# Optimization experiments

Measured on AMD Instinct MI355X. Metric: run time of the kernel, lower is better.

The kernel has to match this reference:

```python
import jax, jax.numpy as jnp
import numpy as np

V, C, T, H, L, B = 32000, 1024, 1024, 16, 8, 4
HS = C // H
STD = 0.02


def _layernorm(x, g, b, eps=1e-5):
    m = jnp.mean(x, axis=-1, keepdims=True)
    v = jnp.mean(jnp.square(x - m), axis=-1, keepdims=True)
    return (x - m) * jax.lax.rsqrt(v + eps) * g + b


def setup_inputs() -> dict:
    key = jax.random.key(0)
    ks = jax.random.split(key, 16)
    n = lambda k, shape: (jax.random.normal(k, shape, dtype=jnp.float32) * STD)
    return {
        "index": jax.random.randint(ks[0], (B, T), 0, V),
        "targets": jax.random.randint(ks[1], (B, T), 0, V),
        "tok_emb": n(ks[2], (V, C)),
        "pos_emb": n(ks[3], (T, C)),
        "wq": n(ks[4], (L, C, C)),
        "wk": n(ks[5], (L, C, C)),
        "wv": n(ks[6], (L, C, C)),
        "wo": n(ks[7], (L, C, C)),
        "bo": jnp.zeros((L, C), jnp.float32),
        "w1": n(ks[8], (L, C, 4 * C)),
        "b1": jnp.zeros((L, 4 * C), jnp.float32),
        "w2": n(ks[9], (L, 4 * C, C)),
        "b2": jnp.zeros((L, C), jnp.float32),
        "ln1_g": jnp.ones((L, C), jnp.float32),
        "ln1_b": jnp.zeros((L, C), jnp.float32),
        "ln2_g": jnp.ones((L, C), jnp.float32),
        "ln2_b": jnp.zeros((L, C), jnp.float32),
        "lnf_g": jnp.ones((C,), jnp.float32),
        "lnf_b": jnp.zeros((C,), jnp.float32),
        "lm_w": n(ks[10], (C, V)),
        "lm_b": jnp.zeros((V,), jnp.float32),
    }


def reference(index, targets, tok_emb, pos_emb, wq, wk, wv, wo, bo, w1, b1, w2,
              b2, ln1_g, ln1_b, ln2_g, ln2_b, lnf_g, lnf_b, lm_w, lm_b):
    b, t = index.shape
    x = tok_emb[index] + pos_emb[:t]                      # [B,T,C]
    causal = jnp.tril(jnp.ones((t, t), dtype=bool))       # tril mask
    scale = HS ** -0.5
    for l in range(L):  # fixed small layer loop
        q = (x @ wq[l]).reshape(b, t, H, HS)
        k = (x @ wk[l]).reshape(b, t, H, HS)
        v = (x @ wv[l]).reshape(b, t, H, HS)
        scores = jnp.einsum('bqhd,bkhd->bhqk', q, k) * scale
        scores = jnp.where(causal, scores, -jnp.inf)
        w = jax.nn.softmax(scores, axis=-1)               # dropout p=0 -> identity
        att = jnp.einsum('bhqk,bkhd->bqhd', w, v).reshape(b, t, C)
        x = _layernorm(x + att @ wo[l] + bo[l], ln1_g[l], ln1_b[l])
        h = jax.nn.relu(x @ w1[l] + b1[l])
        x = _layernorm(x + h @ w2[l] + b2[l], ln2_g[l], ln2_b[l])
    x = _layernorm(x, lnf_g, lnf_b)
    logits = (x @ lm_w + lm_b).reshape(b * t, V)
    logp = jax.nn.log_softmax(logits, axis=-1)
    loss = -jnp.take_along_axis(logp, targets.reshape(-1, 1), axis=1).mean()
    return logits, loss
```

## Files before the change

### kernel.cpp

```cpp
#include <hip/hip_runtime.h>

typedef unsigned short u16;
typedef __attribute__((ext_vector_type(4))) float f32x4;
typedef __attribute__((ext_vector_type(8))) short s16x8;
typedef __attribute__((ext_vector_type(4))) short s16x4;

static constexpr int V = 32000;
static constexpr int C = 1024;
static constexpr int T = 1024;
static constexpr int H = 16;
static constexpr int L = 8;
static constexpr int B = 4;
static constexpr int HS = 64;
static constexpr int BT = B * T;
static constexpr int C4 = 4 * C;
static constexpr int C3 = 3 * C;

__device__ __forceinline__ u16 f2bf(float f) {
  union { float f; unsigned u; } v; v.f = f;
  unsigned r = v.u + 0x7fffu + ((v.u >> 16) & 1u);
  return (u16)(r >> 16);
}

__device__ __forceinline__ void gload16(const u16* g, u16* l) {
  __builtin_amdgcn_global_load_lds(
      (const __attribute__((address_space(1))) void*)g,
      (__attribute__((address_space(3))) void*)l, 16, 0, 0);
}

__device__ __forceinline__ float blockReduceSum(float v) {
  __shared__ float red[4];
  int lane = threadIdx.x & 63, w = threadIdx.x >> 6;
#pragma unroll
  for (int m = 32; m >= 1; m >>= 1) v += __shfl_xor(v, m, 64);
  if (lane == 0) red[w] = v;
  __syncthreads();
  float r = red[0] + red[1] + red[2] + red[3];
  __syncthreads();
  return r;
}

__global__ __launch_bounds__(256) void k_embed(
    const int* __restrict__ idx, const float* __restrict__ tok,
    const float* __restrict__ pos, float* __restrict__ x, u16* __restrict__ xb) {
  int bt = blockIdx.x;
  int t = bt & (T - 1);
  int row = idx[bt];
  const float* te = tok + (size_t)row * C;
  const float* pe = pos + (size_t)t * C;
  float* xo = x + (size_t)bt * C;
  u16* xbo = xb + (size_t)bt * C;
  for (int c = threadIdx.x; c < C; c += 256) {
    float v = te[c] + pe[c];
    xo[c] = v;
    xbo[c] = f2bf(v);
  }
}

__global__ __launch_bounds__(256) void k_transpose(
    const float* __restrict__ W, u16* __restrict__ Wt, int K, int N,
    size_t sW, size_t sWt) {
  __shared__ float tile[64][65];
  const float* Wz = W + sW * blockIdx.z;
  u16* Wtz = Wt + sWt * blockIdx.z;
  int n0 = blockIdx.x * 64, k0 = blockIdx.y * 64;
  int tc = threadIdx.x & 63, tr = threadIdx.x >> 6;
#pragma unroll
  for (int i = 0; i < 16; ++i) {
    int r = tr + i * 4;
    tile[r][tc] = Wz[(size_t)(k0 + r) * N + (n0 + tc)];
  }
  __syncthreads();
#pragma unroll
  for (int i = 0; i < 16; ++i) {
    int r = tr + i * 4;
    Wtz[(size_t)(n0 + r) * K + (k0 + tc)] = f2bf(tile[tc][r]);
  }
}

template <int OUT_BF16, int RELU, int HAS_BIAS, int HAS_RES>
__global__ __launch_bounds__(256, 2) void k_gemm(
    const u16* __restrict__ A, const u16* __restrict__ Bt,
    const float* __restrict__ bias, const float* __restrict__ Res,
    float* __restrict__ Cf, u16* __restrict__ Cb, int M, int N, int K) {
  __shared__ u16 As[128 * 32];
  __shared__ u16 Bs[128 * 32];
  int tid = threadIdx.x;
  int lane = tid & 63, wid = tid >> 6;
  int lm = lane & 15, lg = lane >> 4;
  int wm = wid >> 1, wn = wid & 1;

  unsigned nbx = gridDim.x;
  unsigned nwg = nbx * gridDim.y;
  unsigned orig = blockIdx.y * nbx + blockIdx.x;
  unsigned f = ((nwg & 7u) == 0u) ? (orig & 7u) * (nwg >> 3) + (orig >> 3) : orig;
  int mb = (int)(f / nbx) * 128, nb = (int)(f % nbx) * 128;

  f32x4 acc[4][4];
#pragma unroll
  for (int i = 0; i < 4; ++i)
#pragma unroll
    for (int j = 0; j < 4; ++j) acc[i][j] = f32x4{0.f, 0.f, 0.f, 0.f};

  int r0 = tid >> 2, q0 = tid & 3;
  int r1 = (256 + tid) >> 2, q1 = tid & 3;
  const u16* a0 = A + (size_t)(mb + r0) * K + q0 * 8;
  const u16* a1 = A + (size_t)(mb + r1) * K + q1 * 8;
  const u16* b0 = Bt + (size_t)(nb + r0) * K + q0 * 8;
  const u16* b1 = Bt + (size_t)(nb + r1) * K + q1 * 8;
  u16* lA0 = &As[wid * 512];
  u16* lA1 = &As[2048 + wid * 512];
  u16* lB0 = &Bs[wid * 512];
  u16* lB1 = &Bs[2048 + wid * 512];

  int nK = K >> 5;
  for (int kb = 0; kb < nK; ++kb) {
    __syncthreads();
    int ko = kb * 32;
    gload16(a0 + ko, lA0);
    gload16(a1 + ko, lA1);
    gload16(b0 + ko, lB0);
    gload16(b1 + ko, lB1);
    __syncthreads();
    s16x8 af[4], bfr[4];
#pragma unroll
    for (int m = 0; m < 4; ++m)
      af[m] = *(const s16x8*)&As[(wm * 64 + m * 16 + lm) * 32 + lg * 8];
#pragma unroll
    for (int n = 0; n < 4; ++n)
      bfr[n] = *(const s16x8*)&Bs[(wn * 64 + n * 16 + lm) * 32 + lg * 8];
#pragma unroll
    for (int m = 0; m < 4; ++m)
#pragma unroll
      for (int n = 0; n < 4; ++n)
        acc[m][n] = __builtin_amdgcn_mfma_f32_16x16x32_bf16(af[m], bfr[n],
                                                            acc[m][n], 0, 0, 0);
  }
#pragma unroll
  for (int m = 0; m < 4; ++m) {
#pragma unroll
    for (int n = 0; n < 4; ++n) {
      int col = nb + wn * 64 + n * 16 + lm;
      float bv = HAS_BIAS ? bias[col] : 0.0f;
#pragma unroll
      for (int r = 0; r < 4; ++r) {
        int row = mb + wm * 64 + m * 16 + lg * 4 + r;
        float v = acc[m][n][r] + bv;
        if (HAS_RES) v += Res[(size_t)row * N + col];
        if (RELU) v = v > 0.f ? v : 0.f;
        if (OUT_BF16)
          Cb[(size_t)row * N + col] = f2bf(v);
        else
          Cf[(size_t)row * N + col] = v;
      }
    }
  }
}

template <int OUT_BF16, int RELU, int HAS_BIAS, int HAS_RES, int VT, int LOSS>
__global__ __launch_bounds__(512) void k_gemm256(
    const u16* __restrict__ A, const u16* __restrict__ Bt,
    const float* __restrict__ bias, const float* __restrict__ Res,
    float* __restrict__ Cf, u16* __restrict__ Cb, u16* __restrict__ Vtp,
    float2* __restrict__ Pp, int M, int N, int K) {
  __shared__ u16 As[2][16384];
  __shared__ u16 Bs[2][16384];
  const int tid = threadIdx.x;
  const int lane = tid & 63, wid = tid >> 6;
  const int lm = lane & 15, lg = lane >> 4;
  const int wr = wid >> 2, wc = wid & 3;

  unsigned nbx = gridDim.x;
  unsigned nwg = nbx * gridDim.y;
  unsigned orig = blockIdx.y * nbx + blockIdx.x;
  unsigned f = ((nwg & 7u) == 0u) ? (orig & 7u) * (nwg >> 3) + (orig >> 3) : orig;
  const int mb = (int)(f / nbx) * 256, nb = (int)(f % nbx) * 256;

  int aoff[4], boff[4], ldso[4];
#pragma unroll
  for (int h = 0; h < 4; ++h) {
    const int kk = h >> 1, p = h & 1;
    int rem = p * 512 + tid;
    int rblk = rem >> 6;
    int rem2 = rem & 63;
    int row16 = rem2 >> 2, psl = rem2 & 3;
    int sl = psl ^ ((row16 >> 1) & 3);
    int grow = rblk * 16 + row16;
    int gk = kk * 32 + sl * 8;
    aoff[h] = (mb + grow) * K + gk;
    boff[h] = (nb + grow) * K + gk;
    ldso[h] = kk * 8192 + p * 4096 + wid * 512;
  }
  const int lo = lm * 32 + ((lg ^ ((lm >> 1) & 3)) << 3);

  f32x4 acc[8][4];
#pragma unroll
  for (int i = 0; i < 8; ++i)
#pragma unroll
    for (int j = 0; j < 4; ++j) acc[i][j] = f32x4{0.f, 0.f, 0.f, 0.f};

  const int nK = K >> 6;
  gload16(A + aoff[0], &As[0][ldso[0]]);
  gload16(A + aoff[1], &As[0][ldso[1]]);
  gload16(Bt + boff[0], &Bs[0][ldso[0]]);
  gload16(Bt + boff[1], &Bs[0][ldso[1]]);
  gload16(A + aoff[2], &As[0][ldso[2]]);
  gload16(A + aoff[3], &As[0][ldso[3]]);
  gload16(Bt + boff[2], &Bs[0][ldso[2]]);
  gload16(Bt + boff[3], &Bs[0][ldso[3]]);
  asm volatile("s_waitcnt vmcnt(4)" ::: "memory");
  __builtin_amdgcn_s_barrier();

  for (int t = 0; t < nK; ++t) {
    const int buf = t & 1, nbuf = buf ^ 1;
    const bool pre = (t + 1 < nK);
    const int nk64 = (t + 1) * 64;
    s16x8 af[4], bfr[4];
#pragma unroll
    for (int m = 0; m < 4; ++m)
      af[m] = *(const s16x8*)&As[buf][(wr * 8 + m) * 512 + lo];
#pragma unroll
    for (int n = 0; n < 4; ++n)
      bfr[n] = *(const s16x8*)&Bs[buf][(wc * 4 + n) * 512 + lo];
    if (pre) {
      gload16(A + aoff[0] + nk64, &As[nbuf][ldso[0]]);
      gload16(A + aoff[1] + nk64, &As[nbuf][ldso[1]]);
    }
    __builtin_amdgcn_s_barrier();
    __builtin_amdgcn_s_setprio(1);
#pragma unroll
    for (int m = 0; m < 4; ++m)
#pragma unroll
      for (int n = 0; n < 4; ++n)
        acc[m][n] = __builtin_amdgcn_mfma_f32_16x16x32_bf16(af[m], bfr[n],
                                                            acc[m][n], 0, 0, 0);
    __builtin_amdgcn_s_setprio(0);
    __builtin_amdgcn_s_barrier();
#pragma unroll
    for (int m = 0; m < 4; ++m)
      af[m] = *(const s16x8*)&As[buf][(wr * 8 + 4 + m) * 512 + lo];
    if (pre) {
      gload16(Bt + boff[0] + nk64, &Bs[nbuf][ldso[0]]);
      gload16(Bt + boff[1] + nk64, &Bs[nbuf][ldso[1]]);
    }
    __builtin_amdgcn_s_barrier();
    __builtin_amdgcn_s_setprio(1);
#pragma unroll
    for (int m = 0; m < 4; ++m)
#pragma unroll
      for (int n = 0; n < 4; ++n)
        acc[m + 4][n] = __builtin_amdgcn_mfma_f32_16x16x32_bf16(
            af[m], bfr[n], acc[m + 4][n], 0, 0, 0);
    __builtin_amdgcn_s_setprio(0);
    __builtin_amdgcn_s_barrier();
#pragma unroll
    for (int m = 0; m < 4; ++m)
      af[m] = *(const s16x8*)&As[buf][8192 + (wr * 8 + m) * 512 + lo];
#pragma unroll
    for (int n = 0; n < 4; ++n)
      bfr[n] = *(const s16x8*)&Bs[buf][8192 + (wc * 4 + n) * 512 + lo];
    if (pre) {
      gload16(A + aoff[2] + nk64, &As[nbuf][ldso[2]]);
      gload16(A + aoff[3] + nk64, &As[nbuf][ldso[3]]);
      asm volatile("s_waitcnt vmcnt(6)" ::: "memory");
    } else {
      asm volatile("s_waitcnt vmcnt(0)" ::: "memory");
    }
    __builtin_amdgcn_s_barrier();
    __builtin_amdgcn_s_setprio(1);
#pragma unroll
    for (int m = 0; m < 4; ++m)
#pragma unroll
      for (int n = 0; n < 4; ++n)
        acc[m][n] = __builtin_amdgcn_mfma_f32_16x16x32_bf16(af[m], bfr[n],
                                                            acc[m][n], 0, 0, 0);
    __builtin_amdgcn_s_setprio(0);
    __builtin_amdgcn_s_barrier();
#pragma unroll
    for (int m = 0; m < 4; ++m)
      af[m] = *(const s16x8*)&As[buf][8192 + (wr * 8 + 4 + m) * 512 + lo];
    if (pre) {
      gload16(Bt + boff[2] + nk64, &Bs[nbuf][ldso[2]]);
      gload16(Bt + boff[3] + nk64, &Bs[nbuf][ldso[3]]);
      asm volatile("s_waitcnt vmcnt(4)" ::: "memory");
    }
    __builtin_amdgcn_s_barrier();
    __builtin_amdgcn_s_setprio(1);
#pragma unroll
    for (int m = 0; m < 4; ++m)
#pragma unroll
      for (int n = 0; n < 4; ++n)
        acc[m + 4][n] = __builtin_amdgcn_mfma_f32_16x16x32_bf16(
            af[m], bfr[n], acc[m + 4][n], 0, 0, 0);
    __builtin_amdgcn_s_setprio(0);
    __builtin_amdgcn_s_barrier();
  }
  if (VT && nb >= 2 * C) {
    int hh = ((nb - 2 * C) >> 6) + wc;
#pragma unroll
    for (int m = 0; m < 8; ++m) {
      int t0 = mb + wr * 128 + m * 16 + lg * 4;
      int bb = t0 >> 10, tt = t0 & (T - 1);
      size_t vbase = ((size_t)(bb * H + hh) * HS) * T + tt;
#pragma unroll
      for (int n = 0; n < 4; ++n) {
        int d = n * 16 + lm;
        s16x4 pk;
#pragma unroll
        for (int r = 0; r < 4; ++r) pk[r] = (short)f2bf(acc[m][n][r]);
        *(s16x4*)&Vtp[vbase + (size_t)d * T] = pk;
      }
    }
    return;
  }
  float bv[4];
#pragma unroll
  for (int n = 0; n < 4; ++n)
    bv[n] = HAS_BIAS ? bias[nb + wc * 64 + n * 16 + lm] : 0.0f;
#pragma unroll
  for (int m = 0; m < 8; ++m) {
#pragma unroll
    for (int r = 0; r < 4; ++r) {
      int row = mb + wr * 128 + m * 16 + lg * 4 + r;
#pragma unroll
      for (int n = 0; n < 4; ++n) {
        int col = nb + wc * 64 + n * 16 + lm;
        float v = acc[m][n][r] + bv[n];
        if (HAS_RES) v += Res[(size_t)row * N + col];
        if (RELU) v = v > 0.f ? v : 0.f;
        if (OUT_BF16)
          Cb[(size_t)row * N + col] = f2bf(v);
        else
          Cf[(size_t)row * N + col] = v;
      }
    }
  }
  if (LOSS) {
    __syncthreads();
    float* red = (float*)&As[0][0];
    float Mx[8][4], Sx[8][4];
#pragma unroll
    for (int m = 0; m < 8; ++m)
#pragma unroll
      for (int r = 0; r < 4; ++r) {
        float v0 = acc[m][0][r] + bv[0];
        float v1 = acc[m][1][r] + bv[1];
        float v2 = acc[m][2][r] + bv[2];
        float v3 = acc[m][3][r] + bv[3];
        Mx[m][r] = fmaxf(fmaxf(v0, v1), fmaxf(v2, v3));
      }
#pragma unroll
    for (int d = 1; d < 16; d <<= 1)
#pragma unroll
      for (int m = 0; m < 8; ++m)
#pragma unroll
        for (int r = 0; r < 4; ++r)
          Mx[m][r] = fmaxf(Mx[m][r], __shfl_xor(Mx[m][r], d, 16));
    if (lm == 0) {
#pragma unroll
      for (int m = 0; m < 8; ++m)
#pragma unroll
        for (int r = 0; r < 4; ++r)
          red[(wr * 128 + m * 16 + lg * 4 + r) * 4 + wc] = Mx[m][r];
    }
    __syncthreads();
#pragma unroll
    for (int m = 0; m < 8; ++m)
#pragma unroll
      for (int r = 0; r < 4; ++r) {
        int rl = wr * 128 + m * 16 + lg * 4 + r;
        Mx[m][r] = fmaxf(fmaxf(red[rl * 4 + 0], red[rl * 4 + 1]),
                         fmaxf(red[rl * 4 + 2], red[rl * 4 + 3]));
      }
    __syncthreads();
#pragma unroll
    for (int m = 0; m < 8; ++m)
#pragma unroll
      for (int r = 0; r < 4; ++r)
        Sx[m][r] = __expf(acc[m][0][r] + bv[0] - Mx[m][r]) +
                   __expf(acc[m][1][r] + bv[1] - Mx[m][r]) +
                   __expf(acc[m][2][r] + bv[2] - Mx[m][r]) +
                   __expf(acc[m][3][r] + bv[3] - Mx[m][r]);
#pragma unroll
    for (int d = 1; d < 16; d <<= 1)
#pragma unroll
      for (int m = 0; m < 8; ++m)
#pragma unroll
        for (int r = 0; r < 4; ++r)
          Sx[m][r] += __shfl_xor(Sx[m][r], d, 16);
    if (lm == 0) {
#pragma unroll
      for (int m = 0; m < 8; ++m)
#pragma unroll
        for (int r = 0; r < 4; ++r)
          red[(wr * 128 + m * 16 + lg * 4 + r) * 4 + wc] = Sx[m][r];
    }
    __syncthreads();
    if (wc == 0 && lm == 0) {
      int nblk = nb >> 8;
#pragma unroll
      for (int m = 0; m < 8; ++m)
#pragma unroll
        for (int r = 0; r < 4; ++r) {
          int rl = wr * 128 + m * 16 + lg * 4 + r;
          float ss = red[rl * 4 + 0] + red[rl * 4 + 1] + red[rl * 4 + 2] +
                     red[rl * 4 + 3];
          Pp[(size_t)(mb + rl) * 128 + nblk] = float2{Mx[m][r], ss};
        }
    }
  }
}

__global__ __launch_bounds__(256) void k_attn(
    const u16* __restrict__ qkv, const u16* __restrict__ vt,
    u16* __restrict__ o) {
  constexpr int PP = 72;
  __shared__ u16 Ks[64 * 64];
  __shared__ u16 Vs[64 * 64];
  __shared__ u16 Ps[4][16 * PP];
  int bid = blockIdx.x;
  int p = bid & 7, h = (bid >> 3) & 15, b = bid >> 7;
  int tid = threadIdx.x, lane = tid & 63, wid = tid >> 6;
  int lm = lane & 15, lg = lane >> 4;
  const size_t rowbase = (size_t)b * T * C3 + (size_t)h * HS;
  const u16* kbase = qkv + rowbase + C;
  const u16* vbase = vt + (size_t)(b * H + h) * HS * T;
  const size_t obase = (size_t)b * T * C + (size_t)h * HS;
  const float scale = 0.125f;
  const int sr = tid >> 3, scs = (tid & 7) ^ (sr & 7);
  const int swz0 = (lg ^ (lm & 7)) * 8;
  const int swz1 = ((4 + lg) ^ (lm & 7)) * 8;

  for (int qi = 0; qi < 2; ++qi) {
    int qt = qi ? (15 - p) : p;
    int qw = qt * 64 + wid * 16;
    s16x8 qf[2];
#pragma unroll
    for (int s = 0; s < 2; ++s)
      qf[s] = *(const s16x8*)&qkv[rowbase + (size_t)(qw + lm) * C3 + s * 32 +
                                  lg * 8];
    float m_[4], l_[4];
    f32x4 oacc[4];
#pragma unroll
    for (int r = 0; r < 4; ++r) { m_[r] = -3e38f; l_[r] = 0.f; }
#pragma unroll
    for (int n = 0; n < 4; ++n) oacc[n] = f32x4{0.f, 0.f, 0.f, 0.f};

    for (int kt = 0; kt <= qt; ++kt) {
      __syncthreads();
      gload16(kbase + (size_t)(kt * 64 + sr) * C3 + scs * 8, &Ks[wid * 512]);
      gload16(kbase + (size_t)(kt * 64 + sr + 32) * C3 + scs * 8,
              &Ks[2048 + wid * 512]);
      gload16(vbase + (size_t)sr * T + kt * 64 + scs * 8, &Vs[wid * 512]);
      gload16(vbase + (size_t)(sr + 32) * T + kt * 64 + scs * 8,
              &Vs[2048 + wid * 512]);
      __syncthreads();

      f32x4 s[4];
#pragma unroll
      for (int ch = 0; ch < 4; ++ch) {
        s16x8 k0 = *(const s16x8*)&Ks[(ch * 16 + lm) * 64 + swz0];
        s16x8 k1 = *(const s16x8*)&Ks[(ch * 16 + lm) * 64 + swz1];
        s[ch] = f32x4{0.f, 0.f, 0.f, 0.f};
        s[ch] = __builtin_amdgcn_mfma_f32_16x16x32_bf16(qf[0], k0, s[ch], 0, 0, 0);
        s[ch] = __builtin_amdgcn_mfma_f32_16x16x32_bf16(qf[1], k1, s[ch], 0, 0, 0);
      }
      if (kt == qt) {
#pragma unroll
        for (int ch = 0; ch < 4; ++ch) {
          int col = kt * 64 + ch * 16 + lm;
#pragma unroll
          for (int r = 0; r < 4; ++r) {
            int row = qw + lg * 4 + r;
            s[ch][r] = (col <= row) ? s[ch][r] * scale : -3e38f;
          }
        }
      } else {
#pragma unroll
        for (int ch = 0; ch < 4; ++ch)
#pragma unroll
          for (int r = 0; r < 4; ++r) s[ch][r] *= scale;
      }
      float rmax[4];
#pragma unroll
      for (int r = 0; r < 4; ++r)
        rmax[r] = fmaxf(fmaxf(s[0][r], s[1][r]), fmaxf(s[2][r], s[3][r]));
#pragma unroll
      for (int mm = 1; mm < 16; mm <<= 1)
#pragma unroll
        for (int r = 0; r < 4; ++r)
          rmax[r] = fmaxf(rmax[r], __shfl_xor(rmax[r], mm, 16));
      float alpha[4], rsum[4];
#pragma unroll
      for (int r = 0; r < 4; ++r) {
        float mn = fmaxf(m_[r], rmax[r]);
        alpha[r] = __expf(m_[r] - mn);
        m_[r] = mn;
        rsum[r] = 0.f;
      }
#pragma unroll
      for (int ch = 0; ch < 4; ++ch)
#pragma unroll
        for (int r = 0; r < 4; ++r) {
          float e = __expf(s[ch][r] - m_[r]);
          s[ch][r] = e;
          rsum[r] += e;
        }
#pragma unroll
      for (int mm = 1; mm < 16; mm <<= 1)
#pragma unroll
        for (int r = 0; r < 4; ++r) rsum[r] += __shfl_xor(rsum[r], mm, 16);
#pragma unroll
      for (int r = 0; r < 4; ++r) l_[r] = l_[r] * alpha[r] + rsum[r];
#pragma unroll
      for (int n = 0; n < 4; ++n)
#pragma unroll
        for (int r = 0; r < 4; ++r) oacc[n][r] *= alpha[r];
#pragma unroll
      for (int r = 0; r < 4; ++r) {
        int pr = lg * 4 + r;
#pragma unroll
        for (int ch = 0; ch < 4; ++ch)
          Ps[wid][pr * PP + ch * 16 + lm] = f2bf(s[ch][r]);
      }
      s16x8 pa0 = *(const s16x8*)&Ps[wid][lm * PP + lg * 8];
      s16x8 pa1 = *(const s16x8*)&Ps[wid][lm * PP + 32 + lg * 8];
#pragma unroll
      for (int n = 0; n < 4; ++n) {
        s16x8 v0 = *(const s16x8*)&Vs[(n * 16 + lm) * 64 + swz0];
        s16x8 v1 = *(const s16x8*)&Vs[(n * 16 + lm) * 64 + swz1];
        oacc[n] =
            __builtin_amdgcn_mfma_f32_16x16x32_bf16(pa0, v0, oacc[n], 0, 0, 0);
        oacc[n] =
            __builtin_amdgcn_mfma_f32_16x16x32_bf16(pa1, v1, oacc[n], 0, 0, 0);
      }
    }
    float inv[4];
#pragma unroll
    for (int r = 0; r < 4; ++r) inv[r] = 1.0f / l_[r];
#pragma unroll
    for (int n = 0; n < 4; ++n)
#pragma unroll
      for (int r = 0; r < 4; ++r)
        o[obase + (size_t)(qw + lg * 4 + r) * C + n * 16 + lm] =
            f2bf(oacc[n][r] * inv[r]);
  }
}

__global__ __launch_bounds__(256) void k_ln(
    const float* __restrict__ in, const float* __restrict__ g,
    const float* __restrict__ bsh, float* __restrict__ xout,
    u16* __restrict__ xbout) {
  int row = blockIdx.x;
  const float* xr = in + (size_t)row * C;
  int tid = threadIdx.x;
  float vals[4];
  float s = 0.f;
#pragma unroll
  for (int i = 0; i < 4; ++i) {
    float vv = xr[tid + i * 256];
    vals[i] = vv;
    s += vv;
  }
  s = blockReduceSum(s);
  float mean = s * (1.0f / C);
  float s2 = 0.f;
#pragma unroll
  for (int i = 0; i < 4; ++i) {
    float d = vals[i] - mean;
    s2 += d * d;
  }
  s2 = blockReduceSum(s2);
  float rstd = rsqrtf(s2 * (1.0f / C) + 1e-5f);
#pragma unroll
  for (int i = 0; i < 4; ++i) {
    int c = tid + i * 256;
    float y = (vals[i] - mean) * rstd * g[c] + bsh[c];
    xout[(size_t)row * C + c] = y;
    xbout[(size_t)row * C + c] = f2bf(y);
  }
}

__global__ __launch_bounds__(128) void k_rowloss2(
    const float2* __restrict__ pairs, const float* __restrict__ logits,
    const int* __restrict__ tgt, float* __restrict__ rowloss) {
  int row = blockIdx.x;
  int tid = threadIdx.x;
  float m = -3e38f, s = 0.f;
  if (tid < 125) {
    float2 pv = pairs[(size_t)row * 128 + tid];
    m = pv.x;
    s = pv.y;
  }
#pragma unroll
  for (int d = 1; d < 64; d <<= 1) {
    float mo = __shfl_xor(m, d, 64), so = __shfl_xor(s, d, 64);
    float mn = fmaxf(m, mo);
    s = s * __expf(m - mn) + so * __expf(mo - mn);
    m = mn;
  }
  __shared__ float sm[2], ss[2];
  if ((tid & 63) == 0) { sm[tid >> 6] = m; ss[tid >> 6] = s; }
  __syncthreads();
  if (tid == 0) {
    float M = fmaxf(sm[0], sm[1]);
    float S = ss[0] * __expf(sm[0] - M) + ss[1] * __expf(sm[1] - M);
    rowloss[row] = (M + logf(S)) - logits[(size_t)row * V + tgt[row]];
  }
}

__global__ __launch_bounds__(256) void k_lossreduce(
    const float* __restrict__ rowloss, float* __restrict__ out) {
  __shared__ float red[256];
  int tid = threadIdx.x;
  float s = 0.f;
  for (int i = tid; i < BT; i += 256) s += rowloss[i];
  red[tid] = s;
  __syncthreads();
  for (int m = 128; m >= 1; m >>= 1) {
    if (tid < m) red[tid] += red[tid + m];
    __syncthreads();
  }
  if (tid == 0) out[0] = red[0] * (1.0f / BT);
}

extern "C" void kernel_launch(void* const* d_in, const int* in_sizes, int n_in,
                              void* d_out, int out_size, void* d_ws,
                              size_t ws_size, hipStream_t stream) {
  (void)in_sizes; (void)n_in; (void)out_size; (void)ws_size;
  const int* index = (const int*)d_in[0];
  const int* targets = (const int*)d_in[1];
  const float* tok_emb = (const float*)d_in[2];
  const float* pos_emb = (const float*)d_in[3];
  const float* wq = (const float*)d_in[4];
  const float* wk = (const float*)d_in[5];
  const float* wv = (const float*)d_in[6];
  const float* wo = (const float*)d_in[7];
  const float* bo = (const float*)d_in[8];
  const float* w1 = (const float*)d_in[9];
  const float* b1 = (const float*)d_in[10];
  const float* w2 = (const float*)d_in[11];
  const float* b2 = (const float*)d_in[12];
  const float* ln1_g = (const float*)d_in[13];
  const float* ln1_b = (const float*)d_in[14];
  const float* ln2_g = (const float*)d_in[15];
  const float* ln2_b = (const float*)d_in[16];
  const float* lnf_g = (const float*)d_in[17];
  const float* lnf_b = (const float*)d_in[18];
  const float* lm_w = (const float*)d_in[19];
  const float* lm_b = (const float*)d_in[20];

  float* logits = (float*)d_out;
  float* loss = logits + (size_t)BT * V;

  size_t off = 0;
  auto alloc = [&](size_t bytes) -> void* {
    off = (off + 255) & ~(size_t)255;
    void* p = (void*)((char*)d_ws + off);
    off += bytes;
    return p;
  };
  u16* wqkv_t = (u16*)alloc((size_t)L * C3 * C * 2);
  u16* wo_t = (u16*)alloc((size_t)L * C * C * 2);
  u16* w1_t = (u16*)alloc((size_t)L * C * C4 * 2);
  u16* w2_t = (u16*)alloc((size_t)L * C4 * C * 2);
  u16* lmw_t = (u16*)alloc((size_t)V * C * 2);
  float* x = (float*)alloc((size_t)BT * C * 4);
  float* tmp = (float*)alloc((size_t)BT * C * 4);
  u16* xb = (u16*)alloc((size_t)BT * C * 2);
  u16* qkvb = (u16*)alloc((size_t)BT * C3 * 2);
  u16* vtb = (u16*)alloc((size_t)BT * C * 2);
  u16* attb = (u16*)alloc((size_t)BT * C * 2);
  u16* hb = (u16*)alloc((size_t)BT * C4 * 2);
  float* rowloss = (float*)alloc((size_t)BT * 4);
  float2* pairs = (float2*)alloc((size_t)BT * 128 * 8);

  dim3 blk(256);
  dim3 blk5(512);
  k_transpose<<<dim3(C / 64, C / 64, L), blk, 0, stream>>>(
      wq, wqkv_t, C, C, (size_t)C * C, (size_t)C3 * C);
  k_transpose<<<dim3(C / 64, C / 64, L), blk, 0, stream>>>(
      wk, wqkv_t + (size_t)C * C, C, C, (size_t)C * C, (size_t)C3 * C);
  k_transpose<<<dim3(C / 64, C / 64, L), blk, 0, stream>>>(
      wv, wqkv_t + (size_t)2 * C * C, C, C, (size_t)C * C, (size_t)C3 * C);
  k_transpose<<<dim3(C / 64, C / 64, L), blk, 0, stream>>>(
      wo, wo_t, C, C, (size_t)C * C, (size_t)C * C);
  k_transpose<<<dim3(C4 / 64, C / 64, L), blk, 0, stream>>>(
      w1, w1_t, C, C4, (size_t)C * C4, (size_t)C * C4);
  k_transpose<<<dim3(C / 64, C4 / 64, L), blk, 0, stream>>>(
      w2, w2_t, C4, C, (size_t)C4 * C, (size_t)C4 * C);
  k_transpose<<<dim3(V / 64, C / 64, 1), blk, 0, stream>>>(
      lm_w, lmw_t, C, V, 0, 0);

  k_embed<<<BT, blk, 0, stream>>>(index, tok_emb, pos_emb, x, xb);

  dim3 gQKV(C3 / 256, BT / 256);
  dim3 gCC(C / 128, BT / 128);
  dim3 gC4(C4 / 256, BT / 256);
  for (int l = 0; l < L; ++l) {
    const u16* wqkvt = wqkv_t + (size_t)l * C3 * C;
    const u16* wot = wo_t + (size_t)l * C * C;
    const u16* w1t = w1_t + (size_t)l * C * C4;
    const u16* w2t = w2_t + (size_t)l * C4 * C;

    k_gemm256<1, 0, 0, 0, 1, 0><<<gQKV, blk5, 0, stream>>>(
        xb, wqkvt, nullptr, nullptr, nullptr, qkvb, vtb, nullptr, BT, C3, C);
    k_attn<<<B * H * 8, blk, 0, stream>>>(qkvb, vtb, attb);
    k_gemm<0, 0, 1, 1><<<gCC, blk, 0, stream>>>(
        attb, wot, bo + (size_t)l * C, x, tmp, nullptr, BT, C, C);
    k_ln<<<BT, blk, 0, stream>>>(tmp, ln1_g + (size_t)l * C,
                                 ln1_b + (size_t)l * C, x, xb);
    k_gemm256<1, 1, 1, 0, 0, 0><<<gC4, blk5, 0, stream>>>(
        xb, w1t, b1 + (size_t)l * C4, nullptr, nullptr, hb, nullptr, nullptr,
        BT, C4, C);
    k_gemm<0, 0, 1, 1><<<gCC, blk, 0, stream>>>(
        hb, w2t, b2 + (size_t)l * C, x, tmp, nullptr, BT, C, C4);
    k_ln<<<BT, blk, 0, stream>>>(tmp, ln2_g + (size_t)l * C,
                                 ln2_b + (size_t)l * C, x, xb);
  }
  k_ln<<<BT, blk, 0, stream>>>(x, lnf_g, lnf_b, x, xb);
  k_gemm256<0, 0, 1, 0, 0, 1><<<dim3(V / 256, BT / 256), blk5, 0, stream>>>(
      xb, lmw_t, lm_b, nullptr, logits, nullptr, nullptr, pairs, BT, V, C);
  k_rowloss2<<<BT, dim3(128), 0, stream>>>(pairs, logits, targets, rowloss);
  k_lossreduce<<<1, blk, 0, stream>>>(rowloss, loss);
}
```

Measured before the change: 2.719 ms.

## Double-buffer attention K/V tiles, vectorize embed/layernorm, restructure loss partial reduction

Attention now double-buffers K and V tiles in shared memory, prefetching the next tile while computing on the current one, using explicit vmcnt waits and raw barriers. The embed and layernorm kernels switch to 128-bit vector loads and stores per thread. The LM-head loss epilogue keeps separate max and sum scratch, drops one barrier, lets all 256 threads write per-row partials, and stores those partials block-major so both the writes and the rowloss reads are coalesced. The risks are the extra shared memory and the hand-counted vmcnt, which assumes gload16 issues exactly one memory op per call.

```diff
diff --git a/kernel.cpp b/kernel.cpp
--- a/kernel.cpp
+++ b/kernel.cpp
@@ -46,15 +46,18 @@
   int bt = blockIdx.x;
   int t = bt & (T - 1);
   int row = idx[bt];
-  const float* te = tok + (size_t)row * C;
-  const float* pe = pos + (size_t)t * C;
-  float* xo = x + (size_t)bt * C;
-  u16* xbo = xb + (size_t)bt * C;
-  for (int c = threadIdx.x; c < C; c += 256) {
-    float v = te[c] + pe[c];
-    xo[c] = v;
-    xbo[c] = f2bf(v);
-  }
+  int tid = threadIdx.x;
+  f32x4 tv = ((const f32x4*)(tok + (size_t)row * C))[tid];
+  f32x4 pv = ((const f32x4*)(pos + (size_t)t * C))[tid];
+  f32x4 y;
+  s16x4 yb;
+#pragma unroll
+  for (int j = 0; j < 4; ++j) {
+    y[j] = tv[j] + pv[j];
+    yb[j] = (short)f2bf(y[j]);
+  }
+  ((f32x4*)(x + (size_t)bt * C))[tid] = y;
+  ((s16x4*)(xb + (size_t)bt * C))[tid] = yb;
 }
 
 __global__ __launch_bounds__(256) void k_transpose(
@@ -337,8 +340,9 @@
   }
   if (LOSS) {
     __syncthreads();
-    float* red = (float*)&As[0][0];
-    float Mx[8][4], Sx[8][4];
+    float* redM = (float*)&As[0][0];
+    float* redS = redM + 1024;
+    float Mx[8][4];
 #pragma unroll
     for (int m = 0; m < 8; ++m)
 #pragma unroll
@@ -361,26 +365,22 @@
       for (int m = 0; m < 8; ++m)
 #pragma unroll
         for (int r = 0; r < 4; ++r)
-          red[(wr * 128 + m * 16 + lg * 4 + r) * 4 + wc] = Mx[m][r];
+          redM[(wr * 128 + m * 16 + lg * 4 + r) * 4 + wc] = Mx[m][r];
     }
     __syncthreads();
+    float Sx[8][4];
 #pragma unroll
     for (int m = 0; m < 8; ++m)
 #pragma unroll
       for (int r = 0; r < 4; ++r) {
         int rl = wr * 128 + m * 16 + lg * 4 + r;
-        Mx[m][r] = fmaxf(fmaxf(red[rl * 4 + 0], red[rl * 4 + 1]),
-                         fmaxf(red[rl * 4 + 2], red[rl * 4 + 3]));
-      }
-    __syncthreads();
-#pragma unroll
-    for (int m = 0; m < 8; ++m)
-#pragma unroll
-      for (int r = 0; r < 4; ++r)
-        Sx[m][r] = __expf(acc[m][0][r] + bv[0] - Mx[m][r]) +
-                   __expf(acc[m][1][r] + bv[1] - Mx[m][r]) +
-                   __expf(acc[m][2][r] + bv[2] - Mx[m][r]) +
-                   __expf(acc[m][3][r] + bv[3] - Mx[m][r]);
+        float mm = fmaxf(fmaxf(redM[rl * 4 + 0], redM[rl * 4 + 1]),
+                         fmaxf(redM[rl * 4 + 2], redM[rl * 4 + 3]));
+        Sx[m][r] = __expf(acc[m][0][r] + bv[0] - mm) +
+                   __expf(acc[m][1][r] + bv[1] - mm) +
+                   __expf(acc[m][2][r] + bv[2] - mm) +
+                   __expf(acc[m][3][r] + bv[3] - mm);
+      }
 #pragma unroll
     for (int d = 1; d < 16; d <<= 1)
 #pragma unroll
@@ -393,20 +393,15 @@
       for (int m = 0; m < 8; ++m)
 #pragma unroll
         for (int r = 0; r < 4; ++r)
-          red[(wr * 128 + m * 16 + lg * 4 + r) * 4 + wc] = Sx[m][r];
+          redS[(wr * 128 + m * 16 + lg * 4 + r) * 4 + wc] = Sx[m][r];
     }
     __syncthreads();
-    if (wc == 0 && lm == 0) {
-      int nblk = nb >> 8;
-#pragma unroll
-      for (int m = 0; m < 8; ++m)
-#pragma unroll
-        for (int r = 0; r < 4; ++r) {
-          int rl = wr * 128 + m * 16 + lg * 4 + r;
-          float ss = red[rl * 4 + 0] + red[rl * 4 + 1] + red[rl * 4 + 2] +
-                     red[rl * 4 + 3];
-          Pp[(size_t)(mb + rl) * 128 + nblk] = float2{Mx[m][r], ss};
-        }
+    if (tid < 256) {
+      float mrow = fmaxf(fmaxf(redM[tid * 4 + 0], redM[tid * 4 + 1]),
+                         fmaxf(redM[tid * 4 + 2], redM[tid * 4 + 3]));
+      float srow = redS[tid * 4 + 0] + redS[tid * 4 + 1] + redS[tid * 4 + 2] +
+                   redS[tid * 4 + 3];
+      Pp[(size_t)(nb >> 8) * M + mb + tid] = float2{mrow, srow};
     }
   }
 }
@@ -415,8 +410,8 @@
     const u16* __restrict__ qkv, const u16* __restrict__ vt,
     u16* __restrict__ o) {
   constexpr int PP = 72;
-  __shared__ u16 Ks[64 * 64];
-  __shared__ u16 Vs[64 * 64];
+  __shared__ u16 Ks[2][64 * 64];
+  __shared__ u16 Vs[2][64 * 64];
   __shared__ u16 Ps[4][16 * PP];
   int bid = blockIdx.x;
   int p = bid & 7, h = (bid >> 3) & 15, b = bid >> 7;
@@ -446,21 +441,34 @@
 #pragma unroll
     for (int n = 0; n < 4; ++n) oacc[n] = f32x4{0.f, 0.f, 0.f, 0.f};
 
+    gload16(kbase + (size_t)sr * C3 + scs * 8, &Ks[0][wid * 512]);
+    gload16(kbase + (size_t)(sr + 32) * C3 + scs * 8, &Ks[0][2048 + wid * 512]);
+    gload16(vbase + (size_t)sr * T + scs * 8, &Vs[0][wid * 512]);
+    gload16(vbase + (size_t)(sr + 32) * T + scs * 8, &Vs[0][2048 + wid * 512]);
+
     for (int kt = 0; kt <= qt; ++kt) {
-      __syncthreads();
-      gload16(kbase + (size_t)(kt * 64 + sr) * C3 + scs * 8, &Ks[wid * 512]);
-      gload16(kbase + (size_t)(kt * 64 + sr + 32) * C3 + scs * 8,
-              &Ks[2048 + wid * 512]);
-      gload16(vbase + (size_t)sr * T + kt * 64 + scs * 8, &Vs[wid * 512]);
-      gload16(vbase + (size_t)(sr + 32) * T + kt * 64 + scs * 8,
-              &Vs[2048 + wid * 512]);
-      __syncthreads();
+      int buf = kt & 1;
+      bool pre = kt < qt;
+      if (pre) {
+        int nk = (kt + 1) * 64;
+        int nbuf = buf ^ 1;
+        gload16(kbase + (size_t)(nk + sr) * C3 + scs * 8, &Ks[nbuf][wid * 512]);
+        gload16(kbase + (size_t)(nk + sr + 32) * C3 + scs * 8,
+                &Ks[nbuf][2048 + wid * 512]);
+        gload16(vbase + (size_t)sr * T + nk + scs * 8, &Vs[nbuf][wid * 512]);
+        gload16(vbase + (size_t)(sr + 32) * T + nk + scs * 8,
+                &Vs[nbuf][2048 + wid * 512]);
+        asm volatile("s_waitcnt vmcnt(4)" ::: "memory");
+      } else {
+        asm volatile("s_waitcnt vmcnt(0)" ::: "memory");
+      }
+      __builtin_amdgcn_s_barrier();
 
       f32x4 s[4];
 #pragma unroll
       for (int ch = 0; ch < 4; ++ch) {
-        s16x8 k0 = *(const s16x8*)&Ks[(ch * 16 + lm) * 64 + swz0];
-        s16x8 k1 = *(const s16x8*)&Ks[(ch * 16 + lm) * 64 + swz1];
+        s16x8 k0 = *(const s16x8*)&Ks[buf][(ch * 16 + lm) * 64 + swz0];
+        s16x8 k1 = *(const s16x8*)&Ks[buf][(ch * 16 + lm) * 64 + swz1];
         s[ch] = f32x4{0.f, 0.f, 0.f, 0.f};
         s[ch] = __builtin_amdgcn_mfma_f32_16x16x32_bf16(qf[0], k0, s[ch], 0, 0, 0);
         s[ch] = __builtin_amdgcn_mfma_f32_16x16x32_bf16(qf[1], k1, s[ch], 0, 0, 0);
@@ -527,13 +535,14 @@
       s16x8 pa1 = *(const s16x8*)&Ps[wid][lm * PP + 32 + lg * 8];
 #pragma unroll
       for (int n = 0; n < 4; ++n) {
-        s16x8 v0 = *(const s16x8*)&Vs[(n * 16 + lm) * 64 + swz0];
-        s16x8 v1 = *(const s16x8*)&Vs[(n * 16 + lm) * 64 + swz1];
+        s16x8 v0 = *(const s16x8*)&Vs[buf][(n * 16 + lm) * 64 + swz0];
+        s16x8 v1 = *(const s16x8*)&Vs[buf][(n * 16 + lm) * 64 + swz1];
         oacc[n] =
             __builtin_amdgcn_mfma_f32_16x16x32_bf16(pa0, v0, oacc[n], 0, 0, 0);
         oacc[n] =
             __builtin_amdgcn_mfma_f32_16x16x32_bf16(pa1, v1, oacc[n], 0, 0, 0);
       }
+      __builtin_amdgcn_s_barrier();
     }
     float inv[4];
 #pragma unroll
@@ -552,33 +561,30 @@
     const float* __restrict__ bsh, float* __restrict__ xout,
     u16* __restrict__ xbout) {
   int row = blockIdx.x;
-  const float* xr = in + (size_t)row * C;
   int tid = threadIdx.x;
-  float vals[4];
-  float s = 0.f;
-#pragma unroll
-  for (int i = 0; i < 4; ++i) {
-    float vv = xr[tid + i * 256];
-    vals[i] = vv;
-    s += vv;
-  }
+  f32x4 v = ((const f32x4*)(in + (size_t)row * C))[tid];
+  float s = v[0] + v[1] + v[2] + v[3];
   s = blockReduceSum(s);
   float mean = s * (1.0f / C);
   float s2 = 0.f;
 #pragma unroll
-  for (int i = 0; i < 4; ++i) {
-    float d = vals[i] - mean;
+  for (int j = 0; j < 4; ++j) {
+    float d = v[j] - mean;
     s2 += d * d;
   }
   s2 = blockReduceSum(s2);
   float rstd = rsqrtf(s2 * (1.0f / C) + 1e-5f);
-#pragma unroll
-  for (int i = 0; i < 4; ++i) {
-    int c = tid + i * 256;
-    float y = (vals[i] - mean) * rstd * g[c] + bsh[c];
-    xout[(size_t)row * C + c] = y;
-    xbout[(size_t)row * C + c] = f2bf(y);
-  }
+  f32x4 gv = ((const f32x4*)g)[tid];
+  f32x4 bv = ((const f32x4*)bsh)[tid];
+  f32x4 y;
+  s16x4 yb;
+#pragma unroll
+  for (int j = 0; j < 4; ++j) {
+    y[j] = (v[j] - mean) * rstd * gv[j] + bv[j];
+    yb[j] = (short)f2bf(y[j]);
+  }
+  ((f32x4*)(xout + (size_t)row * C))[tid] = y;
+  ((s16x4*)(xbout + (size_t)row * C))[tid] = yb;
 }
 
 __global__ __launch_bounds__(128) void k_rowloss2(
@@ -588,7 +594,7 @@
   int tid = threadIdx.x;
   float m = -3e38f, s = 0.f;
   if (tid < 125) {
-    float2 pv = pairs[(size_t)row * 128 + tid];
+    float2 pv = pairs[(size_t)tid * BT + row];
     m = pv.x;
     s = pv.y;
   }
```

Result: no change. 2.680 ms (-1.4%).
